# Kernel optimization log

Hardware: AMD Instinct MI355X
Metric: run time of the kernel (lower is better)

## Reference

```python
import jax, jax.numpy as jnp
import numpy as np
from jax import lax


def _ema_gain(g0, rest):
    # g0: [B,1], rest: [B,T-1,1]; g[n] = 0.9*g[n-1] + 0.1*x[n]
    def step(carry, xt):
        g = carry * 0.9 + xt * 0.1
        return g, g
    _, gs = lax.scan(step, g0, jnp.swapaxes(rest, 0, 1))  # gs: [T-1,B,1]
    return jnp.swapaxes(gs, 0, 1)


def setup_inputs() -> dict:
    key = jax.random.key(0)
    mag = jax.random.uniform(key, (48, 5000, 161), dtype=jnp.float32)
    return {"mag": mag}


def reference(mag):
    # mag: [B, T, F] one-sided magnitude spectrum (F = 161 bins of a 320-pt FFT)
    spec_pow = mag ** 2
    # total power: interior bins counted twice, DC and Nyquist once, /320
    sp = ((spec_pow[..., 1:-1] * 2).sum(-1) + spec_pow[..., 0] + spec_pow[..., -1]) / 320.0
    x = jnp.sqrt(sp)[..., None]  # [B, T, 1]
    # single-pole EMA over frames; frame 0 passes through unchanged
    gains = _ema_gain(x[:, 0], x[:, 1:])
    slice_gain = jnp.concatenate([x[:, :1], gains], axis=1)  # [B, T, 1]
    new_mag = mag / (slice_gain + 0.001)
    return (new_mag, slice_gain)
```

## Files before the change

### kernel.cpp

```cpp
#include <hip/hip_runtime.h>

#define NB 48
#define NT 5000
#define NF 161
#define NROWS (NB * NT)
#define MAGN  (NROWS * NF)

typedef float vf4 __attribute__((ext_vector_type(4)));

__global__ __launch_bounds__(256) void x_kernel(const float* __restrict__ mag,
                                                float* __restrict__ gout) {
    __shared__ float sx[16 * NF];
    const int tid  = threadIdx.x;
    const int wave = tid >> 6;
    const int lane = tid & 63;
    const size_t blk_base = (size_t)blockIdx.x * (16 * NF);

    const float4* gp4 = (const float4*)(mag + blk_base);
    float4* sp4 = (float4*)sx;
#pragma unroll
    for (int j = 0; j < 3; ++j) {
        int i4 = tid + 256 * j;
        if (i4 < (16 * NF) / 4) sp4[i4] = gp4[i4];
    }
    __syncthreads();

#pragma unroll
    for (int i = 0; i < 4; ++i) {
        const int r = wave * 4 + i;
        const float* rp = sx + r * NF;
        float sum = 0.f;
#pragma unroll
        for (int k0 = 0; k0 < NF; k0 += 64) {
            int k = k0 + lane;
            if (k < NF) {
                float v = rp[k];
                float w = (k == 0 || k == NF - 1) ? 1.f : 2.f;
                sum += w * v * v;
            }
        }
#pragma unroll
        for (int off = 32; off > 0; off >>= 1)
            sum += __shfl_down(sum, off, 64);
        if (lane == 0)
            gout[blockIdx.x * 16 + r] = sqrtf(sum / 320.f);
    }
}

__global__ __launch_bounds__(256) void scan_kernel(float* __restrict__ gbuf) {
    __shared__ float sx[NT];
    __shared__ float sA[256];
    __shared__ float sB[256];
    const int b   = blockIdx.x;
    const int tid = threadIdx.x;
    float* gp = gbuf + (size_t)b * NT;

    for (int t = tid; t < NT; t += 256) sx[t] = gp[t];
    __syncthreads();

    const int LEN   = 20;
    const int start = 1 + tid * LEN;
    const int end   = min(NT, start + LEN);

    float A = 1.f, Bc = 0.f;
    for (int t = start; t < end; ++t) {
        A  *= 0.9f;
        Bc  = 0.9f * Bc + 0.1f * sx[t];
    }
    sA[tid] = A; sB[tid] = Bc;
    __syncthreads();

    for (int off = 1; off < 256; off <<= 1) {
        float a = sA[tid], bb = sB[tid];
        float ap = 1.f, bp = 0.f;
        if (tid >= off) { ap = sA[tid - off]; bp = sB[tid - off]; }
        __syncthreads();
        sA[tid] = a * ap;
        sB[tid] = a * bp + bb;
        __syncthreads();
    }

    float Ap = 1.f, Bp = 0.f;
    if (tid > 0) { Ap = sA[tid - 1]; Bp = sB[tid - 1]; }
    float g = Ap * sx[0] + Bp;

    if (tid == 0) gp[0] = sx[0];
    for (int t = start; t < end; ++t) {
        g = 0.9f * g + 0.1f * sx[t];
        gp[t] = g;
    }
}

__global__ __launch_bounds__(256) void div_kernel(const float* __restrict__ mag,
                                                  const float* __restrict__ gain,
                                                  float* __restrict__ out) {
    const unsigned n4 = MAGN / 4u;
    const unsigned i4 = blockIdx.x * 256u + threadIdx.x;
    if (i4 >= n4) return;

    const vf4* mag4 = (const vf4*)mag;
    vf4* out4 = (vf4*)out;

    vf4 m = __builtin_nontemporal_load(&mag4[i4]);
    const unsigned base = i4 * 4u;
    const unsigned row0 = base / NF;
    const unsigned row3 = (base + 3u) / NF;
    const float ga = __builtin_amdgcn_rcpf(gain[row0] + 0.001f);
    const float gb = __builtin_amdgcn_rcpf(gain[row3] + 0.001f);
    const unsigned lim = (row0 + 1u) * NF;

    vf4 o;
    o.x = m.x * ga;
    o.y = m.y * ((base + 1u < lim) ? ga : gb);
    o.z = m.z * ((base + 2u < lim) ? ga : gb);
    o.w = m.w * gb;
    __builtin_nontemporal_store(o, &out4[i4]);
}

extern "C" void kernel_launch(void* const* d_in, const int* in_sizes, int n_in,
                              void* d_out, int out_size, void* d_ws, size_t ws_size,
                              hipStream_t stream) {
    const float* mag = (const float*)d_in[0];
    float* out  = (float*)d_out;
    float* gout = out + (size_t)MAGN;

    x_kernel<<<NROWS / 16, 256, 0, stream>>>(mag, gout);
    scan_kernel<<<NB, 256, 0, stream>>>(gout);
    div_kernel<<<(MAGN / 4 + 255) / 256, 256, 0, stream>>>(mag, gout, out);
}
```

Before: 288.8 us.

## Fuse reduction, scan, and divide into one cooperative persistent kernel

Replaces the three separate launches with one cooperative kernel of 1024 persistent blocks. The blocks loop over row groups for the power reduction, grid-sync, run the per-batch scan on 48 blocks, grid-sync again, then do a grid-stride divide pass. The aim is to remove launch gaps and the idle tail between kernels. In exchange, the scan phase leaves most blocks idle behind a grid barrier, and the 20KB of shared memory per block may limit occupancy. If the cooperative launch fails, the code falls back to the original three kernels.

```diff
diff --git a/kernel.cpp b/kernel.cpp
--- a/kernel.cpp
+++ b/kernel.cpp
@@ -1,12 +1,129 @@
 #include <hip/hip_runtime.h>
+#include <hip/hip_cooperative_groups.h>
+
+namespace cg = cooperative_groups;
 
 #define NB 48
 #define NT 5000
 #define NF 161
 #define NROWS (NB * NT)
-#define MAGN  (NROWS * NF)
+#define MAGN  ((size_t)NROWS * NF)
+#define GRID  1024
+#define TPB   256
 
 typedef float vf4 __attribute__((ext_vector_type(4)));
+
+__global__ __launch_bounds__(TPB, 4) void fused_kernel(const float* __restrict__ mag,
+                                                       float* __restrict__ out,
+                                                       float* __restrict__ gout) {
+    cg::grid_group grid = cg::this_grid();
+    __shared__ __align__(16) float sbuf[NT];
+    __shared__ float sA[TPB];
+    __shared__ float sB[TPB];
+
+    const int tid  = threadIdx.x;
+    const int wave = tid >> 6;
+    const int lane = tid & 63;
+
+    for (int g = blockIdx.x; g < NROWS / 16; g += gridDim.x) {
+        const size_t blk_base = (size_t)g * (16 * NF);
+        const float4* gp4 = (const float4*)(mag + blk_base);
+        float4* sp4 = (float4*)sbuf;
+#pragma unroll
+        for (int j = 0; j < 3; ++j) {
+            int i4 = tid + TPB * j;
+            if (i4 < (16 * NF) / 4) sp4[i4] = gp4[i4];
+        }
+        __syncthreads();
+
+#pragma unroll
+        for (int i = 0; i < 4; ++i) {
+            const int r = wave * 4 + i;
+            const float* rp = sbuf + r * NF;
+            float sum = 0.f;
+#pragma unroll
+            for (int k0 = 0; k0 < NF; k0 += 64) {
+                int k = k0 + lane;
+                if (k < NF) {
+                    float v = rp[k];
+                    float w = (k == 0 || k == NF - 1) ? 1.f : 2.f;
+                    sum += w * v * v;
+                }
+            }
+#pragma unroll
+            for (int off = 32; off > 0; off >>= 1)
+                sum += __shfl_down(sum, off, 64);
+            if (lane == 0)
+                gout[g * 16 + r] = sqrtf(sum / 320.f);
+        }
+        __syncthreads();
+    }
+
+    __threadfence();
+    grid.sync();
+
+    if (blockIdx.x < NB) {
+        float* gp = gout + (size_t)blockIdx.x * NT;
+        for (int t = tid; t < NT; t += TPB) sbuf[t] = gp[t];
+        __syncthreads();
+
+        const int LEN   = 20;
+        const int start = 1 + tid * LEN;
+        const int end   = min(NT, start + LEN);
+
+        float A = 1.f, Bc = 0.f;
+        for (int t = start; t < end; ++t) {
+            A  *= 0.9f;
+            Bc  = 0.9f * Bc + 0.1f * sbuf[t];
+        }
+        sA[tid] = A; sB[tid] = Bc;
+        __syncthreads();
+
+        for (int off = 1; off < TPB; off <<= 1) {
+            float a = sA[tid], bb = sB[tid];
+            float ap = 1.f, bp = 0.f;
+            if (tid >= off) { ap = sA[tid - off]; bp = sB[tid - off]; }
+            __syncthreads();
+            sA[tid] = a * ap;
+            sB[tid] = a * bp + bb;
+            __syncthreads();
+        }
+
+        float Ap = 1.f, Bp = 0.f;
+        if (tid > 0) { Ap = sA[tid - 1]; Bp = sB[tid - 1]; }
+        float g = Ap * sbuf[0] + Bp;
+
+        if (tid == 0) gp[0] = sbuf[0];
+        for (int t = start; t < end; ++t) {
+            g = 0.9f * g + 0.1f * sbuf[t];
+            gp[t] = g;
+        }
+    }
+
+    __threadfence();
+    grid.sync();
+
+    const unsigned n4 = (unsigned)(MAGN / 4);
+    const vf4* mag4 = (const vf4*)mag;
+    vf4* out4 = (vf4*)out;
+    for (unsigned i4 = blockIdx.x * (unsigned)TPB + tid; i4 < n4;
+         i4 += gridDim.x * (unsigned)TPB) {
+        vf4 m = __builtin_nontemporal_load(&mag4[i4]);
+        const unsigned base = i4 * 4u;
+        const unsigned row0 = base / NF;
+        const unsigned row3 = (base + 3u) / NF;
+        const float ga = __builtin_amdgcn_rcpf(gout[row0] + 0.001f);
+        const float gb = __builtin_amdgcn_rcpf(gout[row3] + 0.001f);
+        const unsigned lim = (row0 + 1u) * NF;
+
+        vf4 o;
+        o.x = m.x * ga;
+        o.y = m.y * ((base + 1u < lim) ? ga : gb);
+        o.z = m.z * ((base + 2u < lim) ? ga : gb);
+        o.w = m.w * gb;
+        __builtin_nontemporal_store(o, &out4[i4]);
+    }
+}
 
 __global__ __launch_bounds__(256) void x_kernel(const float* __restrict__ mag,
                                                 float* __restrict__ gout) {
@@ -15,7 +132,6 @@
     const int wave = tid >> 6;
     const int lane = tid & 63;
     const size_t blk_base = (size_t)blockIdx.x * (16 * NF);
-
     const float4* gp4 = (const float4*)(mag + blk_base);
     float4* sp4 = (float4*)sx;
 #pragma unroll
@@ -24,7 +140,6 @@
         if (i4 < (16 * NF) / 4) sp4[i4] = gp4[i4];
     }
     __syncthreads();
-
 #pragma unroll
     for (int i = 0; i < 4; ++i) {
         const int r = wave * 4 + i;
@@ -54,14 +169,11 @@
     const int b   = blockIdx.x;
     const int tid = threadIdx.x;
     float* gp = gbuf + (size_t)b * NT;
-
     for (int t = tid; t < NT; t += 256) sx[t] = gp[t];
     __syncthreads();
-
     const int LEN   = 20;
     const int start = 1 + tid * LEN;
     const int end   = min(NT, start + LEN);
-
     float A = 1.f, Bc = 0.f;
     for (int t = start; t < end; ++t) {
         A  *= 0.9f;
@@ -69,7 +181,6 @@
     }
     sA[tid] = A; sB[tid] = Bc;
     __syncthreads();
-
     for (int off = 1; off < 256; off <<= 1) {
         float a = sA[tid], bb = sB[tid];
         float ap = 1.f, bp = 0.f;
@@ -79,11 +190,9 @@
         sB[tid] = a * bp + bb;
         __syncthreads();
     }
-
     float Ap = 1.f, Bp = 0.f;
     if (tid > 0) { Ap = sA[tid - 1]; Bp = sB[tid - 1]; }
     float g = Ap * sx[0] + Bp;
-
     if (tid == 0) gp[0] = sx[0];
     for (int t = start; t < end; ++t) {
         g = 0.9f * g + 0.1f * sx[t];
@@ -94,13 +203,11 @@
 __global__ __launch_bounds__(256) void div_kernel(const float* __restrict__ mag,
                                                   const float* __restrict__ gain,
                                                   float* __restrict__ out) {
-    const unsigned n4 = MAGN / 4u;
+    const unsigned n4 = (unsigned)(MAGN / 4);
     const unsigned i4 = blockIdx.x * 256u + threadIdx.x;
     if (i4 >= n4) return;
-
     const vf4* mag4 = (const vf4*)mag;
     vf4* out4 = (vf4*)out;
-
     vf4 m = __builtin_nontemporal_load(&mag4[i4]);
     const unsigned base = i4 * 4u;
     const unsigned row0 = base / NF;
@@ -108,7 +215,6 @@
     const float ga = __builtin_amdgcn_rcpf(gain[row0] + 0.001f);
     const float gb = __builtin_amdgcn_rcpf(gain[row3] + 0.001f);
     const unsigned lim = (row0 + 1u) * NF;
-
     vf4 o;
     o.x = m.x * ga;
     o.y = m.y * ((base + 1u < lim) ? ga : gb);
@@ -124,7 +230,13 @@
     float* out  = (float*)d_out;
     float* gout = out + (size_t)MAGN;
 
-    x_kernel<<<NROWS / 16, 256, 0, stream>>>(mag, gout);
-    scan_kernel<<<NB, 256, 0, stream>>>(gout);
-    div_kernel<<<(MAGN / 4 + 255) / 256, 256, 0, stream>>>(mag, gout, out);
-}
+    void* args[] = {(void*)&mag, (void*)&out, (void*)&gout};
+    hipError_t e = hipLaunchCooperativeKernel((const void*)fused_kernel,
+                                              dim3(GRID), dim3(TPB),
+                                              args, 0, stream);
+    if (e != hipSuccess) {
+        x_kernel<<<NROWS / 16, 256, 0, stream>>>(mag, gout);
+        scan_kernel<<<NB, 256, 0, stream>>>(gout);
+        div_kernel<<<((unsigned)(MAGN / 4) + 255u) / 256u, 256, 0, stream>>>(mag, gout, out);
+    }
+}
```

After: 627.0 us. +117.1%, slower.
